# Optimization experiments

Hardware: AMD Instinct MI355X
Metric: run time of the kernel (lower is better)

The kernel has to match this reference:

```python
import jax, jax.numpy as jnp
import numpy as np

B, C_IN, H, W = 4, 3, 512, 512
KH = KW = 3
K = KH * KW
C_OUT = 3
HO, WO = H - 2, W - 2  # valid conv, stride 1, no padding


def setup_inputs() -> dict:
    key = jax.random.key(0)
    k1, k2, k3, k4, k5, k6 = jax.random.split(key, 6)
    x = jax.random.normal(k1, (B, C_IN, H, W), dtype=jnp.float32)
    # conv1: Conv2d(3, 18, 3) -> predicts offsets (2*kh*kw = 18 channels)
    w1 = jax.random.normal(k2, (18, C_IN, KH, KW), dtype=jnp.float32) * 0.05
    b1 = jax.random.normal(k3, (18,), dtype=jnp.float32) * 0.05
    # conv2: DeformConv2d(3, 3, 3) weight + bias
    w2 = jax.random.normal(k4, (C_OUT, C_IN, KH, KW), dtype=jnp.float32) * 0.1
    b2 = jax.random.normal(k5, (C_OUT,), dtype=jnp.float32) * 0.1
    return {"x": x, "w1": w1, "b1": b1, "w2": w2, "b2": b2}


def _bilinear_gather(img, y, x):
    # img: [B, C, H, W]; y, x: [B, K, Ho, Wo] float sampling coords.
    # Bilinear interpolation with zeros outside the image (torchvision semantics).
    y0 = jnp.floor(y)
    x0 = jnp.floor(x)
    dy = y - y0
    dx = x - x0
    out = jnp.zeros((img.shape[0], img.shape[1]) + y.shape[1:], dtype=img.dtype)
    for iy, wy in ((y0, 1.0 - dy), (y0 + 1.0, dy)):
        for ix, wx in ((x0, 1.0 - dx), (x0 + 1.0, dx)):
            valid = (iy >= 0) & (iy < H) & (ix >= 0) & (ix < W)
            yi = jnp.clip(iy, 0, H - 1).astype(jnp.int32)
            xi = jnp.clip(ix, 0, W - 1).astype(jnp.int32)
            w = jnp.where(valid, wy * wx, 0.0)  # [B,K,Ho,Wo]
            g = jax.vmap(lambda im, a, b: im[:, a, b])(img, yi, xi)  # [B,C,K,Ho,Wo]
            out = out + g * w[:, None]
    return out


def _forward(x, w1, b1, w2, b2):
    dn = ("NCHW", "OIHW", "NCHW")
    # offset-predicting conv: [B, 18, Ho, Wo]
    offs = jax.lax.conv_general_dilated(x, w1, (1, 1), "VALID", dimension_numbers=dn)
    offs = offs + b1[None, :, None, None]
    # torchvision layout: channel 2k = dy, 2k+1 = dx for kernel tap k (row-major)
    off = offs.reshape(B, K, 2, HO, WO)
    ky = jnp.repeat(jnp.arange(KH, dtype=jnp.float32), KW)  # [K]
    kx = jnp.tile(jnp.arange(KW, dtype=jnp.float32), KH)    # [K]
    gy = jnp.arange(HO, dtype=jnp.float32)[None, None, :, None]
    gx = jnp.arange(WO, dtype=jnp.float32)[None, None, None, :]
    sy = gy + ky[None, :, None, None] + off[:, :, 0]  # [B,K,Ho,Wo]
    sx = gx + kx[None, :, None, None] + off[:, :, 1]
    val = _bilinear_gather(x, sy, sx)  # [B,C,K,Ho,Wo]
    w2r = w2.reshape(C_OUT, C_IN, K)
    out = jnp.einsum("ock,bckij->boij", w2r, val) + b2[None, :, None, None]
    return out


def reference(x, w1, b1, w2, b2):
    return _forward(x, w1, b1, w2, b2)
```

## Files before the change

### kernel.cpp

```cpp
#include <hip/hip_runtime.h>

#define BB 4
#define CIN 3
#define HH 512
#define WW 512
#define KK 9
#define COUT 3
#define HO 510
#define WO 510
#define HW (HH * WW)
#define HOWO (HO * WO)

#define PR 518
#define PC 520
#define PADR 3
#define PADC 4
#define XP_BYTES ((size_t)BB * PR * PC * sizeof(uint2))

typedef __fp16 h2 __attribute__((ext_vector_type(2)));

__device__ __forceinline__ h2 pkrtz(float a, float b) {
    return __builtin_amdgcn_cvt_pkrtz(a, b);
}
__device__ __forceinline__ float fdot2f(h2 a, h2 b, float c) {
    return __builtin_amdgcn_fdot2(a, b, c, false);
}
__device__ __forceinline__ h2 uint_as_h2(unsigned u) {
    return __builtin_bit_cast(h2, u);
}
__device__ __forceinline__ unsigned h2_as_uint(h2 h) {
    return __builtin_bit_cast(unsigned, h);
}
__device__ __forceinline__ float w1e(const float* w1, int ch, int c, int r, int s) {
    return w1[ch * 27 + c * 9 + r * 3 + s];
}

__global__ __launch_bounds__(256) void repack_padh(
    const float* __restrict__ x, uint2* __restrict__ xp)
{
    const int idx = blockIdx.x * blockDim.x + threadIdx.x;
    const int total = BB * PR * PC;
    if (idx >= total) return;
    const int b = idx / (PR * PC);
    const int rem = idx - b * (PR * PC);
    const int y = rem / PC;
    const int xc = rem - y * PC;
    const int ys = y - PADR;
    const int xs = xc - PADC;
    uint2 v = make_uint2(0u, 0u);
    if ((unsigned)ys < (unsigned)HH && (unsigned)xs < (unsigned)WW) {
        const float* xb = x + (size_t)b * CIN * HW;
        const int p = ys * WW + xs;
        v.x = h2_as_uint(pkrtz(xb[p], xb[HW + p]));
        v.y = h2_as_uint(pkrtz(xb[2 * HW + p], 0.f));
    }
    xp[idx] = v;
}

__global__ __launch_bounds__(256) void deform_fused8(
    const uint2* __restrict__ xp,
    const float* __restrict__ w1,
    const float* __restrict__ b1,
    const float* __restrict__ w2,
    const float* __restrict__ b2,
    float* __restrict__ out)
{
    __shared__ uint4 s_w1h[KK * 9];
    __shared__ float s_b[18];
    __shared__ uint4 s_w2a[KK];
    __shared__ uint2 s_w2b[KK];
    __shared__ float s_b2[COUT];

    if (threadIdx.x < KK * 9) {
        const int k = threadIdx.x / 9;
        const int pos = threadIdx.x % 9;
        const int r = pos / 3, s = pos % 3;
        uint4 u;
        u.x = h2_as_uint(pkrtz(w1e(w1, 2 * k, 0, r, s), w1e(w1, 2 * k, 1, r, s)));
        u.y = h2_as_uint(pkrtz(w1e(w1, 2 * k, 2, r, s), 0.f));
        u.z = h2_as_uint(pkrtz(w1e(w1, 2 * k + 1, 0, r, s), w1e(w1, 2 * k + 1, 1, r, s)));
        u.w = h2_as_uint(pkrtz(w1e(w1, 2 * k + 1, 2, r, s), 0.f));
        s_w1h[threadIdx.x] = u;
    }
    if (threadIdx.x < KK) {
        const int k = threadIdx.x;
        uint4 wa;
        wa.x = h2_as_uint(pkrtz(w2[k], w2[9 + k]));
        wa.y = h2_as_uint(pkrtz(w2[18 + k], 0.f));
        wa.z = h2_as_uint(pkrtz(w2[27 + k], w2[36 + k]));
        wa.w = h2_as_uint(pkrtz(w2[45 + k], 0.f));
        s_w2a[k] = wa;
        uint2 wb;
        wb.x = h2_as_uint(pkrtz(w2[54 + k], w2[63 + k]));
        wb.y = h2_as_uint(pkrtz(w2[72 + k], 0.f));
        s_w2b[k] = wb;
    }
    if (threadIdx.x < 18) s_b[threadIdx.x] = b1[threadIdx.x];
    if (threadIdx.x < COUT) s_b2[threadIdx.x] = b2[threadIdx.x];
    __syncthreads();

    constexpr int WP = WO / 2;
    const int idx = blockIdx.x * 256 + threadIdx.x;
    if (idx >= BB * HO * WP) return;
    const int jp = idx % WP;
    const int t1 = idx / WP;
    const int i = t1 % HO;
    const int b = t1 / HO;
    const int j = jp * 2;

    const uint2* xb2 = xp + (size_t)b * (PR * PC);

    h2 p01[3][4], p2p[3][4];
#pragma unroll
    for (int r = 0; r < 3; ++r) {
        const int base = (i + r + PADR) * PC + (j + PADC);
        const uint4 qa = *reinterpret_cast<const uint4*>(xb2 + base);
        const uint4 qb = *reinterpret_cast<const uint4*>(xb2 + base + 2);
        p01[r][0] = uint_as_h2(qa.x); p2p[r][0] = uint_as_h2(qa.y);
        p01[r][1] = uint_as_h2(qa.z); p2p[r][1] = uint_as_h2(qa.w);
        p01[r][2] = uint_as_h2(qb.x); p2p[r][2] = uint_as_h2(qb.y);
        p01[r][3] = uint_as_h2(qb.z); p2p[r][3] = uint_as_h2(qb.w);
    }

    unsigned pk0[KK], pk1[KK];
#pragma unroll
    for (int k = 0; k < KK; ++k) {
        float dy0 = s_b[2 * k], dx0 = s_b[2 * k + 1];
        float dy1 = dy0, dx1 = dx0;
        const uint4* wk = &s_w1h[k * 9];
#pragma unroll
        for (int r = 0; r < 3; ++r)
#pragma unroll
            for (int s = 0; s < 3; ++s) {
                const uint4 wq = wk[r * 3 + s];
                const h2 wy01 = uint_as_h2(wq.x);
                const h2 wy2x = uint_as_h2(wq.y);
                const h2 wx01 = uint_as_h2(wq.z);
                const h2 wx2x = uint_as_h2(wq.w);
                dy0 = fdot2f(wy01, p01[r][s], dy0);
                dy0 = fdot2f(wy2x, p2p[r][s], dy0);
                dx0 = fdot2f(wx01, p01[r][s], dx0);
                dx0 = fdot2f(wx2x, p2p[r][s], dx0);
                dy1 = fdot2f(wy01, p01[r][s + 1], dy1);
                dy1 = fdot2f(wy2x, p2p[r][s + 1], dy1);
                dx1 = fdot2f(wx01, p01[r][s + 1], dx1);
                dx1 = fdot2f(wx2x, p2p[r][s + 1], dx1);
            }
        pk0[k] = h2_as_uint(pkrtz(dy0, dx0));
        pk1[k] = h2_as_uint(pkrtz(dy1, dx1));
    }

    const float fi = (float)(i + PADR);
    const float fj = (float)(j + PADC);
    float acc00 = s_b2[0], acc01 = s_b2[1], acc02 = s_b2[2];
    float acc10 = s_b2[0], acc11 = s_b2[1], acc12 = s_b2[2];

#pragma unroll
    for (int k = 0; k < KK; ++k) {
        const uint4 wa = s_w2a[k];
        const uint2 wb = s_w2b[k];
        const float ry = fi + (float)(k / 3);
        const float rx = fj + (float)(k % 3);

#pragma unroll
        for (int p = 0; p < 2; ++p) {
            const h2 d = uint_as_h2(p ? pk1[k] : pk0[k]);
            const float syp = ry + (float)d.x;
            const float sxp = rx + (float)p + (float)d.y;
            const int y0 = (int)syp;
            const int x0 = (int)sxp;
            const float fy = syp - (float)y0;
            const float fx = sxp - (float)x0;

            const int a00 = y0 * PC + x0;
            const uint2 c00 = xb2[a00];
            const uint2 c01 = xb2[a00 + 1];
            const uint2 c10 = xb2[a00 + PC];
            const uint2 c11 = xb2[a00 + PC + 1];

            const float wy0 = 1.f - fy, wx0 = 1.f - fx;
            const float w00 = wy0 * wx0, w01 = wy0 * fx;
            const float w10 = fy * wx0, w11 = fy * fx;
            const h2 h00 = pkrtz(w00, w00);
            const h2 h01 = pkrtz(w01, w01);
            const h2 h10 = pkrtz(w10, w10);
            const h2 h11 = pkrtz(w11, w11);

            const h2 g00 = uint_as_h2(c00.x), e00 = uint_as_h2(c00.y);
            const h2 g01 = uint_as_h2(c01.x), e01 = uint_as_h2(c01.y);
            const h2 g10 = uint_as_h2(c10.x), e10 = uint_as_h2(c10.y);
            const h2 g11 = uint_as_h2(c11.x), e11 = uint_as_h2(c11.y);

            h2 vg = h00 * g00;
            vg = h01 * g01 + vg;
            vg = h10 * g10 + vg;
            vg = h11 * g11 + vg;
            h2 ve = h00 * e00;
            ve = h01 * e01 + ve;
            ve = h10 * e10 + ve;
            ve = h11 * e11 + ve;

            if (p == 0) {
                acc00 = fdot2f(uint_as_h2(wa.x), vg, fdot2f(uint_as_h2(wa.y), ve, acc00));
                acc01 = fdot2f(uint_as_h2(wa.z), vg, fdot2f(uint_as_h2(wa.w), ve, acc01));
                acc02 = fdot2f(uint_as_h2(wb.x), vg, fdot2f(uint_as_h2(wb.y), ve, acc02));
            } else {
                acc10 = fdot2f(uint_as_h2(wa.x), vg, fdot2f(uint_as_h2(wa.y), ve, acc10));
                acc11 = fdot2f(uint_as_h2(wa.z), vg, fdot2f(uint_as_h2(wa.w), ve, acc11));
                acc12 = fdot2f(uint_as_h2(wb.x), vg, fdot2f(uint_as_h2(wb.y), ve, acc12));
            }
        }
    }

    float* ob = out + (size_t)b * COUT * HOWO + (size_t)i * WO + j;
    {
        float2 st;
        st.x = acc00; st.y = acc10;
        *reinterpret_cast<float2*>(&ob[0 * HOWO]) = st;
        st.x = acc01; st.y = acc11;
        *reinterpret_cast<float2*>(&ob[1 * HOWO]) = st;
        st.x = acc02; st.y = acc12;
        *reinterpret_cast<float2*>(&ob[2 * HOWO]) = st;
    }
}

__global__ __launch_bounds__(256) void deform_fused_kernel(
    const float* __restrict__ x, const float* __restrict__ w1,
    const float* __restrict__ b1, const float* __restrict__ w2,
    const float* __restrict__ b2, float* __restrict__ out)
{
    __shared__ float s_w1[18 * 27];
    __shared__ float s_b1[18];
    __shared__ float s_w2[COUT * CIN * KK];
    __shared__ float s_b2[COUT];
    for (int t = threadIdx.x; t < 18 * 27; t += blockDim.x) s_w1[t] = w1[t];
    if (threadIdx.x < 18) s_b1[threadIdx.x] = b1[threadIdx.x];
    if (threadIdx.x < COUT * CIN * KK) s_w2[threadIdx.x] = w2[threadIdx.x];
    if (threadIdx.x < COUT) s_b2[threadIdx.x] = b2[threadIdx.x];
    __syncthreads();
    const int idx = blockIdx.x * blockDim.x + threadIdx.x;
    if (idx >= BB * HOWO) return;
    const int j = idx % WO;
    const int tmp = idx / WO;
    const int i = tmp % HO;
    const int b = tmp / HO;
    const float* xb = x + (size_t)b * CIN * HW;
    float patch[CIN][3][3];
#pragma unroll
    for (int c = 0; c < CIN; ++c)
#pragma unroll
        for (int r = 0; r < 3; ++r)
#pragma unroll
            for (int s = 0; s < 3; ++s)
                patch[c][r][s] = xb[c * HW + (i + r) * WW + (j + s)];
    float acc0 = s_b2[0], acc1 = s_b2[1], acc2 = s_b2[2];
#pragma unroll
    for (int k = 0; k < KK; ++k) {
        const int ky = k / 3, kx = k % 3;
        float dy = s_b1[2 * k], dx = s_b1[2 * k + 1];
        const float* wy = &s_w1[(2 * k) * 27];
        const float* wx = &s_w1[(2 * k + 1) * 27];
        int t = 0;
#pragma unroll
        for (int c = 0; c < CIN; ++c)
#pragma unroll
            for (int r = 0; r < 3; ++r)
#pragma unroll
                for (int s = 0; s < 3; ++s, ++t) {
                    const float pv = patch[c][r][s];
                    dy += pv * wy[t];
                    dx += pv * wx[t];
                }
        const float sy = (float)(i + ky) + dy;
        const float sx = (float)(j + kx) + dx;
        const float y0f = floorf(sy), x0f = floorf(sx);
        const float fy = sy - y0f, fx = sx - x0f;
        const int y0 = (int)y0f, x0 = (int)x0f;
        float v0 = 0.f, v1 = 0.f, v2 = 0.f;
#pragma unroll
        for (int cy = 0; cy < 2; ++cy) {
            const int iy = y0 + cy;
            const float wyf = cy ? fy : (1.f - fy);
            const bool vy = (iy >= 0) && (iy < HH);
            const int iyc = iy < 0 ? 0 : (iy > HH - 1 ? HH - 1 : iy);
#pragma unroll
            for (int cx = 0; cx < 2; ++cx) {
                const int ix = x0 + cx;
                const float wxf = cx ? fx : (1.f - fx);
                const bool vx = (ix >= 0) && (ix < WW);
                const int ixc = ix < 0 ? 0 : (ix > WW - 1 ? WW - 1 : ix);
                const float wgt = (vy && vx) ? (wyf * wxf) : 0.f;
                const int off = iyc * WW + ixc;
                v0 += wgt * xb[0 * HW + off];
                v1 += wgt * xb[1 * HW + off];
                v2 += wgt * xb[2 * HW + off];
            }
        }
#pragma unroll
        for (int o = 0; o < COUT; ++o) {
            const float c0 = s_w2[(o * CIN + 0) * KK + k];
            const float c1 = s_w2[(o * CIN + 1) * KK + k];
            const float c2 = s_w2[(o * CIN + 2) * KK + k];
            const float contrib = c0 * v0 + c1 * v1 + c2 * v2;
            if (o == 0) acc0 += contrib;
            else if (o == 1) acc1 += contrib;
            else acc2 += contrib;
        }
    }
    float* ob = out + (size_t)b * COUT * HOWO + (size_t)i * WO + j;
    ob[0 * HOWO] = acc0;
    ob[1 * HOWO] = acc1;
    ob[2 * HOWO] = acc2;
}

extern "C" void kernel_launch(void* const* d_in, const int* in_sizes, int n_in,
                              void* d_out, int out_size, void* d_ws, size_t ws_size,
                              hipStream_t stream) {
    const float* x  = (const float*)d_in[0];
    const float* w1 = (const float*)d_in[1];
    const float* b1 = (const float*)d_in[2];
    const float* w2 = (const float*)d_in[3];
    const float* b2 = (const float*)d_in[4];
    float* out = (float*)d_out;

    if (ws_size >= XP_BYTES) {
        uint2* xp = (uint2*)d_ws;
        {
            const int total = BB * PR * PC;
            repack_padh<<<(total + 255) / 256, 256, 0, stream>>>(x, xp);
        }
        {
            const int total = BB * HO * (WO / 2);
            deform_fused8<<<(total + 255) / 256, 256, 0, stream>>>(
                xp, w1, b1, w2, b2, out);
        }
    } else {
        const int total = BB * HOWO;
        deform_fused_kernel<<<(total + 255) / 256, 256, 0, stream>>>(
            x, w1, b1, w2, b2, out);
    }
}
```

Baseline: 39.67 us.

## Process one output pixel per thread and vectorize the fp16 repack kernel

The main deform kernel moves from two output pixels per thread back to one pixel per thread. That doubles the thread count and lowers per-thread register pressure and the serial gather chain, in exchange for more redundant patch loads and scalar stores. The repack kernel now handles two pixels per thread, reading float2 and writing uint4 to cut per-element overhead. The fallback kernel only has whitespace changes.

```diff
diff --git a/kernel.cpp b/kernel.cpp
--- a/kernel.cpp
+++ b/kernel.cpp
@@ -35,29 +35,35 @@
     return w1[ch * 27 + c * 9 + r * 3 + s];
 }
 
-__global__ __launch_bounds__(256) void repack_padh(
+__global__ __launch_bounds__(256) void repack_padh2(
     const float* __restrict__ x, uint2* __restrict__ xp)
 {
+    constexpr int PCH = PC / 2;
     const int idx = blockIdx.x * blockDim.x + threadIdx.x;
-    const int total = BB * PR * PC;
+    const int total = BB * PR * PCH;
     if (idx >= total) return;
-    const int b = idx / (PR * PC);
-    const int rem = idx - b * (PR * PC);
-    const int y = rem / PC;
-    const int xc = rem - y * PC;
+    const int b = idx / (PR * PCH);
+    const int rem = idx - b * (PR * PCH);
+    const int y = rem / PCH;
+    const int q = rem - y * PCH;
     const int ys = y - PADR;
-    const int xs = xc - PADC;
-    uint2 v = make_uint2(0u, 0u);
+    const int xs = 2 * q - PADC;
+    uint4 v = make_uint4(0u, 0u, 0u, 0u);
     if ((unsigned)ys < (unsigned)HH && (unsigned)xs < (unsigned)WW) {
         const float* xb = x + (size_t)b * CIN * HW;
         const int p = ys * WW + xs;
-        v.x = h2_as_uint(pkrtz(xb[p], xb[HW + p]));
-        v.y = h2_as_uint(pkrtz(xb[2 * HW + p], 0.f));
-    }
-    xp[idx] = v;
-}
-
-__global__ __launch_bounds__(256) void deform_fused8(
+        const float2 a0 = *reinterpret_cast<const float2*>(xb + p);
+        const float2 a1 = *reinterpret_cast<const float2*>(xb + HW + p);
+        const float2 a2 = *reinterpret_cast<const float2*>(xb + 2 * HW + p);
+        v.x = h2_as_uint(pkrtz(a0.x, a1.x));
+        v.y = h2_as_uint(pkrtz(a2.x, 0.f));
+        v.z = h2_as_uint(pkrtz(a0.y, a1.y));
+        v.w = h2_as_uint(pkrtz(a2.y, 0.f));
+    }
+    reinterpret_cast<uint4*>(xp)[idx] = v;
+}
+
+__global__ __launch_bounds__(256) void deform_fused9(
     const uint2* __restrict__ xp,
     const float* __restrict__ w1,
     const float* __restrict__ b1,
@@ -99,129 +105,91 @@
     if (threadIdx.x < COUT) s_b2[threadIdx.x] = b2[threadIdx.x];
     __syncthreads();
 
-    constexpr int WP = WO / 2;
     const int idx = blockIdx.x * 256 + threadIdx.x;
-    if (idx >= BB * HO * WP) return;
-    const int jp = idx % WP;
-    const int t1 = idx / WP;
+    if (idx >= BB * HOWO) return;
+    const int j = idx % WO;
+    const int t1 = idx / WO;
     const int i = t1 % HO;
     const int b = t1 / HO;
-    const int j = jp * 2;
 
     const uint2* xb2 = xp + (size_t)b * (PR * PC);
 
-    h2 p01[3][4], p2p[3][4];
-#pragma unroll
-    for (int r = 0; r < 3; ++r) {
-        const int base = (i + r + PADR) * PC + (j + PADC);
-        const uint4 qa = *reinterpret_cast<const uint4*>(xb2 + base);
-        const uint4 qb = *reinterpret_cast<const uint4*>(xb2 + base + 2);
-        p01[r][0] = uint_as_h2(qa.x); p2p[r][0] = uint_as_h2(qa.y);
-        p01[r][1] = uint_as_h2(qa.z); p2p[r][1] = uint_as_h2(qa.w);
-        p01[r][2] = uint_as_h2(qb.x); p2p[r][2] = uint_as_h2(qb.y);
-        p01[r][3] = uint_as_h2(qb.z); p2p[r][3] = uint_as_h2(qb.w);
-    }
-
-    unsigned pk0[KK], pk1[KK];
+    h2 p01[3][3], p2p[3][3];
+#pragma unroll
+    for (int r = 0; r < 3; ++r)
+#pragma unroll
+        for (int s = 0; s < 3; ++s) {
+            const uint2 q = xb2[(i + r + PADR) * PC + (j + s + PADC)];
+            p01[r][s] = uint_as_h2(q.x);
+            p2p[r][s] = uint_as_h2(q.y);
+        }
+
+    unsigned pk[KK];
 #pragma unroll
     for (int k = 0; k < KK; ++k) {
-        float dy0 = s_b[2 * k], dx0 = s_b[2 * k + 1];
-        float dy1 = dy0, dx1 = dx0;
+        float dy = s_b[2 * k], dx = s_b[2 * k + 1];
         const uint4* wk = &s_w1h[k * 9];
 #pragma unroll
         for (int r = 0; r < 3; ++r)
 #pragma unroll
             for (int s = 0; s < 3; ++s) {
                 const uint4 wq = wk[r * 3 + s];
-                const h2 wy01 = uint_as_h2(wq.x);
-                const h2 wy2x = uint_as_h2(wq.y);
-                const h2 wx01 = uint_as_h2(wq.z);
-                const h2 wx2x = uint_as_h2(wq.w);
-                dy0 = fdot2f(wy01, p01[r][s], dy0);
-                dy0 = fdot2f(wy2x, p2p[r][s], dy0);
-                dx0 = fdot2f(wx01, p01[r][s], dx0);
-                dx0 = fdot2f(wx2x, p2p[r][s], dx0);
-                dy1 = fdot2f(wy01, p01[r][s + 1], dy1);
-                dy1 = fdot2f(wy2x, p2p[r][s + 1], dy1);
-                dx1 = fdot2f(wx01, p01[r][s + 1], dx1);
-                dx1 = fdot2f(wx2x, p2p[r][s + 1], dx1);
+                dy = fdot2f(uint_as_h2(wq.x), p01[r][s], dy);
+                dy = fdot2f(uint_as_h2(wq.y), p2p[r][s], dy);
+                dx = fdot2f(uint_as_h2(wq.z), p01[r][s], dx);
+                dx = fdot2f(uint_as_h2(wq.w), p2p[r][s], dx);
             }
-        pk0[k] = h2_as_uint(pkrtz(dy0, dx0));
-        pk1[k] = h2_as_uint(pkrtz(dy1, dx1));
+        pk[k] = h2_as_uint(pkrtz(dy, dx));
     }
 
     const float fi = (float)(i + PADR);
     const float fj = (float)(j + PADC);
-    float acc00 = s_b2[0], acc01 = s_b2[1], acc02 = s_b2[2];
-    float acc10 = s_b2[0], acc11 = s_b2[1], acc12 = s_b2[2];
+    float acc0 = s_b2[0], acc1 = s_b2[1], acc2 = s_b2[2];
 
 #pragma unroll
     for (int k = 0; k < KK; ++k) {
         const uint4 wa = s_w2a[k];
         const uint2 wb = s_w2b[k];
-        const float ry = fi + (float)(k / 3);
-        const float rx = fj + (float)(k % 3);
-
-#pragma unroll
-        for (int p = 0; p < 2; ++p) {
-            const h2 d = uint_as_h2(p ? pk1[k] : pk0[k]);
-            const float syp = ry + (float)d.x;
-            const float sxp = rx + (float)p + (float)d.y;
-            const int y0 = (int)syp;
-            const int x0 = (int)sxp;
-            const float fy = syp - (float)y0;
-            const float fx = sxp - (float)x0;
-
-            const int a00 = y0 * PC + x0;
-            const uint2 c00 = xb2[a00];
-            const uint2 c01 = xb2[a00 + 1];
-            const uint2 c10 = xb2[a00 + PC];
-            const uint2 c11 = xb2[a00 + PC + 1];
-
-            const float wy0 = 1.f - fy, wx0 = 1.f - fx;
-            const float w00 = wy0 * wx0, w01 = wy0 * fx;
-            const float w10 = fy * wx0, w11 = fy * fx;
-            const h2 h00 = pkrtz(w00, w00);
-            const h2 h01 = pkrtz(w01, w01);
-            const h2 h10 = pkrtz(w10, w10);
-            const h2 h11 = pkrtz(w11, w11);
-
-            const h2 g00 = uint_as_h2(c00.x), e00 = uint_as_h2(c00.y);
-            const h2 g01 = uint_as_h2(c01.x), e01 = uint_as_h2(c01.y);
-            const h2 g10 = uint_as_h2(c10.x), e10 = uint_as_h2(c10.y);
-            const h2 g11 = uint_as_h2(c11.x), e11 = uint_as_h2(c11.y);
-
-            h2 vg = h00 * g00;
-            vg = h01 * g01 + vg;
-            vg = h10 * g10 + vg;
-            vg = h11 * g11 + vg;
-            h2 ve = h00 * e00;
-            ve = h01 * e01 + ve;
-            ve = h10 * e10 + ve;
-            ve = h11 * e11 + ve;
-
-            if (p == 0) {
-                acc00 = fdot2f(uint_as_h2(wa.x), vg, fdot2f(uint_as_h2(wa.y), ve, acc00));
-                acc01 = fdot2f(uint_as_h2(wa.z), vg, fdot2f(uint_as_h2(wa.w), ve, acc01));
-                acc02 = fdot2f(uint_as_h2(wb.x), vg, fdot2f(uint_as_h2(wb.y), ve, acc02));
-            } else {
-                acc10 = fdot2f(uint_as_h2(wa.x), vg, fdot2f(uint_as_h2(wa.y), ve, acc10));
-                acc11 = fdot2f(uint_as_h2(wa.z), vg, fdot2f(uint_as_h2(wa.w), ve, acc11));
-                acc12 = fdot2f(uint_as_h2(wb.x), vg, fdot2f(uint_as_h2(wb.y), ve, acc12));
-            }
-        }
+        const h2 d = uint_as_h2(pk[k]);
+        const float syp = fi + (float)(k / 3) + (float)d.x;
+        const float sxp = fj + (float)(k % 3) + (float)d.y;
+        const int y0 = (int)syp;
+        const int x0 = (int)sxp;
+        const float fy = syp - (float)y0;
+        const float fx = sxp - (float)x0;
+
+        const int a00 = y0 * PC + x0;
+        const uint2 c00 = xb2[a00];
+        const uint2 c01 = xb2[a00 + 1];
+        const uint2 c10 = xb2[a00 + PC];
+        const uint2 c11 = xb2[a00 + PC + 1];
+
+        const float wy0 = 1.f - fy, wx0 = 1.f - fx;
+        const float w00 = wy0 * wx0, w01 = wy0 * fx;
+        const float w10 = fy * wx0, w11 = fy * fx;
+        const h2 h00 = pkrtz(w00, w00);
+        const h2 h01 = pkrtz(w01, w01);
+        const h2 h10 = pkrtz(w10, w10);
+        const h2 h11 = pkrtz(w11, w11);
+
+        h2 vg = h00 * uint_as_h2(c00.x);
+        vg = h01 * uint_as_h2(c01.x) + vg;
+        vg = h10 * uint_as_h2(c10.x) + vg;
+        vg = h11 * uint_as_h2(c11.x) + vg;
+        h2 ve = h00 * uint_as_h2(c00.y);
+        ve = h01 * uint_as_h2(c01.y) + ve;
+        ve = h10 * uint_as_h2(c10.y) + ve;
+        ve = h11 * uint_as_h2(c11.y) + ve;
+
+        acc0 = fdot2f(uint_as_h2(wa.x), vg, fdot2f(uint_as_h2(wa.y), ve, acc0));
+        acc1 = fdot2f(uint_as_h2(wa.z), vg, fdot2f(uint_as_h2(wa.w), ve, acc1));
+        acc2 = fdot2f(uint_as_h2(wb.x), vg, fdot2f(uint_as_h2(wb.y), ve, acc2));
     }
 
     float* ob = out + (size_t)b * COUT * HOWO + (size_t)i * WO + j;
-    {
-        float2 st;
-        st.x = acc00; st.y = acc10;
-        *reinterpret_cast<float2*>(&ob[0 * HOWO]) = st;
-        st.x = acc01; st.y = acc11;
-        *reinterpret_cast<float2*>(&ob[1 * HOWO]) = st;
-        st.x = acc02; st.y = acc12;
-        *reinterpret_cast<float2*>(&ob[2 * HOWO]) = st;
-    }
+    ob[0 * HOWO] = acc0;
+    ob[1 * HOWO] = acc1;
+    ob[2 * HOWO] = acc2;
 }
 
 __global__ __launch_bounds__(256) void deform_fused_kernel(
@@ -262,15 +230,15 @@
         const float* wx = &s_w1[(2 * k + 1) * 27];
         int t = 0;
 #pragma unroll
-        for (int c = 0; c < CIN; ++c)
-#pragma unroll
-            for (int r = 0; r < 3; ++r)
-#pragma unroll
-                for (int s = 0; s < 3; ++s, ++t) {
-                    const float pv = patch[c][r][s];
-                    dy += pv * wy[t];
-                    dx += pv * wx[t];
-                }
+    for (int c = 0; c < CIN; ++c)
+#pragma unroll
+        for (int r = 0; r < 3; ++r)
+#pragma unroll
+            for (int s = 0; s < 3; ++s, ++t) {
+                const float pv = patch[c][r][s];
+                dy += pv * wy[t];
+                dx += pv * wx[t];
+            }
         const float sy = (float)(i + ky) + dy;
         const float sx = (float)(j + kx) + dx;
         const float y0f = floorf(sy), x0f = floorf(sx);
@@ -326,12 +294,12 @@
     if (ws_size >= XP_BYTES) {
         uint2* xp = (uint2*)d_ws;
         {
-            const int total = BB * PR * PC;
-            repack_padh<<<(total + 255) / 256, 256, 0, stream>>>(x, xp);
+            const int total = BB * PR * (PC / 2);
+            repack_padh2<<<(total + 255) / 256, 256, 0, stream>>>(x, xp);
         }
         {
-            const int total = BB * HO * (WO / 2);
-            deform_fused8<<<(total + 255) / 256, 256, 0, stream>>>(
+            const int total = BB * HOWO;
+            deform_fused9<<<(total + 255) / 256, 256, 0, stream>>>(
                 xp, w1, b1, w2, b2, out);
         }
     } else {
```

Result: faster. 38.84 us (-2.1%).
